# Kernel tuning notes

Hardware: AMD Instinct MI355X
Metric: run time of the kernel (lower is better)

The kernel has to match this reference:

```python
import jax, jax.numpy as jnp
import numpy as np

B, S, H = 2, 2048, 2048
NQ, NKV, DH = 16, 8, 128
EPS = 1e-6
ROPE_BASE = 10000.0


def setup_inputs() -> dict:
    key = jax.random.key(0)
    ks = jax.random.split(key, 6)
    hidden_states = jax.random.normal(ks[0], (B, S, H), dtype=jnp.float32)
    # real RoPE tables
    inv_freq = 1.0 / (ROPE_BASE ** (jnp.arange(0, DH, 2, dtype=jnp.float32) / DH))
    pos = jnp.arange(S, dtype=jnp.float32)
    freqs = pos[:, None] * inv_freq[None, :]              # [S, DH/2]
    emb = jnp.concatenate([freqs, freqs], axis=-1)        # [S, DH]
    cos = jnp.broadcast_to(jnp.cos(emb)[None], (B, S, DH))
    sin = jnp.broadcast_to(jnp.sin(emb)[None], (B, S, DH))
    # additive causal mask [1,1,S,S]
    causal = jnp.tril(jnp.ones((S, S), dtype=bool))
    attention_mask = jnp.where(causal, 0.0, jnp.finfo(jnp.float32).min)[None, None]
    q_w = jax.random.normal(ks[1], (H, H), dtype=jnp.float32) * 0.02
    k_w = jax.random.normal(ks[2], (NKV * DH, H), dtype=jnp.float32) * 0.02
    v_w = jax.random.normal(ks[3], (NKV * DH, H), dtype=jnp.float32) * 0.02
    o_w = jax.random.normal(ks[4], (H, H), dtype=jnp.float32) * 0.02
    return {"hidden_states": hidden_states, "cos": cos, "sin": sin,
            "attention_mask": attention_mask,
            "q_w": q_w, "k_w": k_w, "v_w": v_w, "o_w": o_w}


def _rotate_half(x):
    x1, x2 = jnp.split(x, 2, axis=-1)
    return jnp.concatenate([-x2, x1], axis=-1)


def _l2norm(x, eps=EPS):
    # weightless RMS norm over head_dim (Llama4TextL2Norm)
    return x * jax.lax.rsqrt(jnp.mean(x * x, axis=-1, keepdims=True) + eps)


def reference(hidden_states, cos, sin, attention_mask, q_w, k_w, v_w, o_w):
    b, s, _ = hidden_states.shape
    # projections (no bias) -> [B, n_heads, S, DH]
    q = jnp.einsum('bsh,dh->bsd', hidden_states, q_w).reshape(b, s, NQ, DH).transpose(0, 2, 1, 3)
    k = jnp.einsum('bsh,dh->bsd', hidden_states, k_w).reshape(b, s, NKV, DH).transpose(0, 2, 1, 3)
    v = jnp.einsum('bsh,dh->bsd', hidden_states, v_w).reshape(b, s, NKV, DH).transpose(0, 2, 1, 3)
    # NanoChat negates sin before standard HF rotary
    sin_e = (-sin)[:, None, :, :]   # [B,1,S,DH]
    cos_e = cos[:, None, :, :]
    q = q * cos_e + _rotate_half(q) * sin_e
    k = k * cos_e + _rotate_half(k) * sin_e
    # weightless QK RMS norm
    q = _l2norm(q)
    k = _l2norm(k)
    # GQA: repeat kv heads
    groups = NQ // NKV
    k = jnp.repeat(k, groups, axis=1)
    v = jnp.repeat(v, groups, axis=1)
    scaling = DH ** -0.5
    scores = jnp.einsum('bhqd,bhkd->bhqk', q, k) * scaling + attention_mask
    probs = jax.nn.softmax(scores, axis=-1)
    attn = jnp.einsum('bhqk,bhkd->bhqd', probs, v)           # [B,H,S,DH]
    attn = attn.transpose(0, 2, 1, 3).reshape(b, s, NQ * DH)
    out = jnp.einsum('bsd,hd->bsh', attn, o_w)
    return out
```

## Files before the change

### kernel.cpp

```cpp
#include <hip/hip_runtime.h>

typedef unsigned short ushort_t;
typedef __bf16 bf16x8 __attribute__((ext_vector_type(8)));
typedef float f32x4 __attribute__((ext_vector_type(4)));
typedef unsigned int u32x4 __attribute__((ext_vector_type(4)));
typedef unsigned short us4 __attribute__((ext_vector_type(4)));
typedef unsigned short us8 __attribute__((ext_vector_type(8)));

#define DEVINL __device__ __forceinline__

DEVINL ushort_t f2bf(float f) {
    unsigned u = __float_as_uint(f);
    u += 0x7FFF + ((u >> 16) & 1);
    return (ushort_t)(u >> 16);
}
DEVINL float bf2f(ushort_t h) { return __uint_as_float(((unsigned)h) << 16); }

DEVINL void gload_lds16(const void* g, void* l) {
    __builtin_amdgcn_global_load_lds(
        (const __attribute__((address_space(1))) void*)g,
        (__attribute__((address_space(3))) void*)l, 16, 0, 0);
}

DEVINL bf16x8 ld_frag(const ushort_t* p) {
    us8 v = *(const us8*)p;
    return __builtin_bit_cast(bf16x8, v);
}

#define BAR()     asm volatile("s_barrier" ::: "memory")
#define LGKM0()   asm volatile("s_waitcnt lgkmcnt(0)" ::: "memory")
#define VMCNT(n)  asm volatile("s_waitcnt vmcnt(" #n ")" ::: "memory")

#define BARRIER_KEEP4()  asm volatile("s_waitcnt vmcnt(4)\n\ts_barrier" ::: "memory")
#define BARRIER_KEEP0()  asm volatile("s_waitcnt vmcnt(0)\n\ts_barrier" ::: "memory")

__global__ __launch_bounds__(256) void convert_all(const f32x4* __restrict__ h,
                                                   const f32x4* __restrict__ qw,
                                                   const f32x4* __restrict__ kw,
                                                   const f32x4* __restrict__ vw,
                                                   const f32x4* __restrict__ ow,
                                                   us4* __restrict__ hb,
                                                   us4* __restrict__ wqkv,
                                                   us4* __restrict__ owb) {
    const int N0 = 2097152;
    const int N1 = 1048576;
    const int N2 = 524288;
    const int N3 = 524288;
    int i = blockIdx.x * 256 + threadIdx.x;
    const f32x4* src; us4* dst;
    if (i < N0)                               { src = h  + i;                 dst = hb + i; }
    else if ((i -= N0) < N1)                  { src = qw + i;                 dst = wqkv + i; }
    else if ((i -= N1) < N2)                  { src = kw + i;                 dst = wqkv + 1048576 + i; }
    else if ((i -= N2) < N3)                  { src = vw + i;                 dst = wqkv + 1572864 + i; }
    else                                      { i -= N3; src = ow + i;       dst = owb + i; }
    f32x4 f = *src;
    us4 o;
    o[0] = f2bf(f[0]); o[1] = f2bf(f[1]); o[2] = f2bf(f[2]); o[3] = f2bf(f[3]);
    *dst = o;
}

template <typename OutT>
__global__ __launch_bounds__(512, 2) void gemm256(const ushort_t* __restrict__ A,
                                                  const ushort_t* __restrict__ W,
                                                  OutT* __restrict__ C,
                                                  int N, int K) {
    __shared__ ushort_t As[2][256 * 64];
    __shared__ ushort_t Bs[2][256 * 64];
    const int t = threadIdx.x;
    const int lane = t & 63;
    const int quad = lane >> 4, l16 = lane & 15;
    const int wm = t >> 8, wn = (t >> 6) & 3;

    int bid = blockIdx.x;
    int xcd = bid & 7, j = bid >> 3;
    int tm, tn;
    if (N == 4096) { tm = (xcd >> 1) * 4 + (j >> 3); tn = (xcd & 1) * 8 + (j & 7); }
    else           { tm = xcd * 2 + (j >> 3);        tn = j & 7; }
    const int bm = tm * 256, bn = tn * 256;

    const int srow0 = t >> 3;
    const int sg0 = ((t & 7) ^ (srow0 & 7)) * 8;
    const int srow1 = srow0 + 64;
    const int sg1 = ((t & 7) ^ (srow1 & 7)) * 8;

    auto stageA = [&](int buf, int half, int k0) {
        gload_lds16(A + (size_t)(bm + half * 128 + srow0) * K + k0 + sg0,
                    &As[buf][half * 8192 + t * 8]);
        gload_lds16(A + (size_t)(bm + half * 128 + srow1) * K + k0 + sg1,
                    &As[buf][half * 8192 + 4096 + t * 8]);
    };
    auto stageB = [&](int buf, int half, int k0) {
        gload_lds16(W + (size_t)(bn + half * 128 + srow0) * K + k0 + sg0,
                    &Bs[buf][half * 8192 + t * 8]);
        gload_lds16(W + (size_t)(bn + half * 128 + srow1) * K + k0 + sg1,
                    &Bs[buf][half * 8192 + 4096 + t * 8]);
    };

    const int xsw = l16 & 7;
    const int arow = (wm * 128 + l16) * 64;
    const int brow = (wn * 64 + l16) * 64;
    const int ac0 = ((0 + quad) ^ xsw) * 8;
    const int ac1 = ((4 + quad) ^ xsw) * 8;

    auto ldA = [&](int buf, int mf, int kk) {
        return ld_frag(&As[buf][arow + mf * 1024 + (kk ? ac1 : ac0)]);
    };
    auto ldB = [&](int buf, int nf, int kk) {
        return ld_frag(&Bs[buf][brow + nf * 1024 + (kk ? ac1 : ac0)]);
    };

    f32x4 acc[8][4];
#pragma unroll
    for (int i = 0; i < 8; i++)
#pragma unroll
        for (int jj = 0; jj < 4; jj++) acc[i][jj] = f32x4{0.f, 0.f, 0.f, 0.f};

    const int NIT = K >> 6;
    stageA(0, 0, 0); stageA(0, 1, 0); stageB(0, 0, 0); stageB(0, 1, 0);
    VMCNT(4);
    stageB(1, 0, 64); stageB(1, 1, 64); stageA(1, 0, 64);
    VMCNT(6);
    BAR();

    bf16x8 a[4][2], b[4][2];
    for (int tt = 0; tt < NIT; ++tt) {
        const int buf = tt & 1;
        const int k2 = (tt + 2) << 6;

#pragma unroll
        for (int mt = 0; mt < 4; mt++) { a[mt][0] = ldA(buf, mt, 0); a[mt][1] = ldA(buf, mt, 1); }
#pragma unroll
        for (int nt = 0; nt < 4; nt++) { b[nt][0] = ldB(buf, nt, 0); b[nt][1] = ldB(buf, nt, 1); }
        if (tt + 1 < NIT) stageA(buf ^ 1, 1, (tt + 1) << 6);
        BAR(); LGKM0();
        __builtin_amdgcn_s_setprio(1);
#pragma unroll
        for (int mt = 0; mt < 4; mt++)
#pragma unroll
            for (int nt = 0; nt < 2; nt++)
#pragma unroll
                for (int kk = 0; kk < 2; kk++)
                    acc[mt][nt] = __builtin_amdgcn_mfma_f32_16x16x32_bf16(a[mt][kk], b[nt][kk], acc[mt][nt], 0, 0, 0);
        __builtin_amdgcn_s_setprio(0);
        LGKM0();
        BAR();

        if (tt + 2 < NIT) stageB(buf, 0, k2);
        BAR();
        __builtin_amdgcn_s_setprio(1);
#pragma unroll
        for (int mt = 0; mt < 4; mt++)
#pragma unroll
            for (int nt = 0; nt < 2; nt++)
#pragma unroll
                for (int kk = 0; kk < 2; kk++)
                    acc[mt][2 + nt] = __builtin_amdgcn_mfma_f32_16x16x32_bf16(a[mt][kk], b[2 + nt][kk], acc[mt][2 + nt], 0, 0, 0);
        __builtin_amdgcn_s_setprio(0);
        BAR();

#pragma unroll
        for (int mt = 0; mt < 4; mt++) { a[mt][0] = ldA(buf, 4 + mt, 0); a[mt][1] = ldA(buf, 4 + mt, 1); }
        if (tt + 2 < NIT) stageB(buf, 1, k2);
        BAR(); LGKM0();
        __builtin_amdgcn_s_setprio(1);
#pragma unroll
        for (int mt = 0; mt < 4; mt++)
#pragma unroll
            for (int nt = 0; nt < 2; nt++)
#pragma unroll
                for (int kk = 0; kk < 2; kk++)
                    acc[4 + mt][nt] = __builtin_amdgcn_mfma_f32_16x16x32_bf16(a[mt][kk], b[nt][kk], acc[4 + mt][nt], 0, 0, 0);
        __builtin_amdgcn_s_setprio(0);
        BAR();

        if (tt + 2 < NIT)      { stageA(buf, 0, k2); VMCNT(6); }
        else if (tt + 1 < NIT) { VMCNT(0); }
        BAR();
        __builtin_amdgcn_s_setprio(1);
#pragma unroll
        for (int mt = 0; mt < 4; mt++)
#pragma unroll
            for (int nt = 0; nt < 2; nt++)
#pragma unroll
                for (int kk = 0; kk < 2; kk++)
                    acc[4 + mt][2 + nt] = __builtin_amdgcn_mfma_f32_16x16x32_bf16(a[mt][kk], b[2 + nt][kk], acc[4 + mt][2 + nt], 0, 0, 0);
        __builtin_amdgcn_s_setprio(0);
        BAR();
    }

#pragma unroll
    for (int mf = 0; mf < 8; mf++)
#pragma unroll
        for (int nf = 0; nf < 4; nf++) {
            const int row = bm + wm * 128 + mf * 16 + quad * 4;
            const int col = bn + wn * 64 + nf * 16 + l16;
#pragma unroll
            for (int rr = 0; rr < 4; rr++) {
                float v = acc[mf][nf][rr];
                if constexpr (sizeof(OutT) == 2)
                    C[(size_t)(row + rr) * N + col] = (OutT)f2bf(v);
                else
                    C[(size_t)(row + rr) * N + col] = v;
            }
        }
}

__global__ __launch_bounds__(256) void rope_norm(const ushort_t* __restrict__ qkv,
                                                 const float* __restrict__ cosb,
                                                 const float* __restrict__ sinb,
                                                 ushort_t* __restrict__ q,
                                                 ushort_t* __restrict__ k) {
    int row = blockIdx.x;
    int b = row >> 11, s = row & 2047;
    int w = threadIdx.x >> 6, lane = threadIdx.x & 63;
    int hh = blockIdx.y * 4 + w;
    const ushort_t* src = qkv + (size_t)row * 4096 + hh * 128;
    float x1 = bf2f(src[lane]);
    float x2 = bf2f(src[lane + 64]);
    float c = cosb[(size_t)row * 128 + lane];
    float sn = sinb[(size_t)row * 128 + lane];
    float y1 = x1 * c + x2 * sn;
    float y2 = x2 * c - x1 * sn;
    float ss = y1 * y1 + y2 * y2;
#pragma unroll
    for (int off = 1; off < 64; off <<= 1) ss += __shfl_xor(ss, off);
    float rinv = rsqrtf(ss * (1.0f / 128.0f) + 1e-6f);
    y1 *= rinv; y2 *= rinv;
    ushort_t* dst;
    if (hh < 16) dst = q + (((size_t)(b * 16 + hh)) * 2048 + s) * 128;
    else         dst = k + (((size_t)(b * 8 + hh - 16)) * 2048 + s) * 128;
    dst[lane] = f2bf(y1);
    dst[lane + 64] = f2bf(y2);
}

__global__ __launch_bounds__(256) void v_transpose(const ushort_t* __restrict__ qkv,
                                                   ushort_t* __restrict__ vt) {
    __shared__ ushort_t tile[64 * 72];
    int t = threadIdx.x;
    int s0 = blockIdx.x * 64, d0 = blockIdx.y * 64, bh = blockIdx.z;
    int b = bh >> 3, kvh = bh & 7;
    {
        int sl = t >> 2, c = t & 3;
        const ushort_t* src = qkv + (size_t)(b * 2048 + s0 + sl) * 4096 + 3072 + kvh * 128 + d0 + c * 16;
        u32x4 v0 = *(const u32x4*)src;
        u32x4 v1 = *(const u32x4*)(src + 8);
        *(u32x4*)&tile[sl * 72 + c * 16] = v0;
        *(u32x4*)&tile[sl * 72 + c * 16 + 8] = v1;
    }
    __syncthreads();
    {
        int dl = t >> 2, c = t & 3;
        alignas(16) ushort_t tmp[16];
#pragma unroll
        for (int i = 0; i < 16; i++) tmp[i] = tile[(c * 16 + i) * 72 + dl];
        ushort_t* dst = vt + (size_t)(bh * 128 + d0 + dl) * 2048 + s0 + c * 16;
        *(u32x4*)dst = *(const u32x4*)&tmp[0];
        *(u32x4*)(dst + 8) = *(const u32x4*)&tmp[8];
    }
}

__global__ __launch_bounds__(512) void flash_attn(const ushort_t* __restrict__ q,
                                                  const ushort_t* __restrict__ k,
                                                  const ushort_t* __restrict__ vt,
                                                  ushort_t* __restrict__ attn) {
    __shared__ ushort_t Ks[3][4 * 64 * 32];
    __shared__ ushort_t Vts[3][2 * 128 * 32];
    __shared__ ushort_t Ps[2 * 64 * 72];
    __shared__ float    Lred[2][4][2][16];
    const int t = threadIdx.x;
    const int w = t >> 6, lane = t & 63;
    const int w4 = w & 3, wh = w >> 2;
    const int quad = lane >> 4, l16 = lane & 15;
    const int sw = (l16 >> 1) & 3;
    const int lid = blockIdx.x;
    const int xcd = lid & 7, jj = lid >> 3;
    const int g = xcd * 2 + (jj >> 4);
    const int p = jj & 15;
    const int b = g >> 3, kvh = g & 7;
    const int h0 = kvh * 2;
    const size_t kbase = ((size_t)(b * 8 + kvh)) * 2048 * 128;
    const size_t vbase = ((size_t)(b * 8 + kvh)) * 128 * 2048;

    const float C1 = 0.12751744f;
    const float C2 = 1.45f;

    auto stage = [&](int j0, int buf) {
#pragma unroll
        for (int i = 0; i < 2; i++) {
            int u = i * 512 + t;
            int qd = u >> 8, rr = (u >> 2) & 63;
            int c4 = ((u & 3) ^ ((rr >> 1) & 3)) * 8;
            gload_lds16(k + kbase + (size_t)(j0 + rr) * 128 + qd * 32 + c4,
                        (char*)Ks[buf] + u * 16);
        }
#pragma unroll
        for (int i = 0; i < 2; i++) {
            int u = i * 512 + t;
            int ks = u >> 9, dd = (u >> 2) & 127;
            int c4 = ((u & 3) ^ ((dd >> 1) & 3)) * 8;
            gload_lds16(vt + vbase + (size_t)dd * 2048 + j0 + ks * 32 + c4,
                        (char*)Vts[buf] + u * 16);
        }
    };

    const int qtile0 = 31 - p;
    const int S_total = qtile0 + 1 + p + 1;
    auto j0_of = [&](int s) { return (s <= qtile0 ? s : s - qtile0 - 1) * 64; };

    stage(j0_of(0), 0);
    stage(j0_of(1), 1);
    int sidx = 0, cb = 0, pb = 2;

    for (int pass = 0; pass < 2; ++pass) {
        const int qi = pass ? p : qtile0;
        const int q0 = qi * 64;

        bf16x8 qf[2][4];
#pragma unroll
        for (int h = 0; h < 2; h++) {
            const size_t qbase = ((size_t)(b * 16 + h0 + h) * 2048 + q0 + w4 * 16 + l16) * 128;
#pragma unroll
            for (int qd = 0; qd < 4; qd++) {
                us8 v = *(const us8*)(q + qbase + qd * 32 + quad * 8);
                qf[h][qd] = __builtin_bit_cast(bf16x8, v);
            }
        }

        f32x4 o[2][4];
#pragma unroll
        for (int h = 0; h < 2; h++)
#pragma unroll
            for (int i = 0; i < 4; i++) o[h][i] = f32x4{0.f, 0.f, 0.f, 0.f};
        float lsum[2][4];
#pragma unroll
        for (int h = 0; h < 2; h++)
#pragma unroll
            for (int r = 0; r < 4; r++) lsum[h][r] = 0.f;

        for (int jt = 0; jt <= qi; ++jt) {
            const int j0 = jt * 64;
            const bool diag = (jt == qi);
            if (sidx + 1 < S_total) BARRIER_KEEP4();
            else                    BARRIER_KEEP0();
            if (sidx + 2 < S_total) stage(j0_of(sidx + 2), pb);
            const ushort_t* Kb = Ks[cb];
            const ushort_t* Vb = Vts[cb];
            cb = cb == 2 ? 0 : cb + 1;
            pb = pb == 2 ? 0 : pb + 1;
            sidx++;

            f32x4 sc[2][2];
#pragma unroll
            for (int h = 0; h < 2; h++)
#pragma unroll
                for (int c = 0; c < 2; c++) sc[h][c] = f32x4{0.f, 0.f, 0.f, 0.f};
            __builtin_amdgcn_s_setprio(1);
#pragma unroll
            for (int c = 0; c < 2; c++)
#pragma unroll
                for (int qd = 0; qd < 4; qd++) {
                    bf16x8 kf = ld_frag(&Kb[qd * 2048 + ((wh * 2 + c) * 16 + l16) * 32 + (quad ^ sw) * 8]);
                    sc[0][c] = __builtin_amdgcn_mfma_f32_16x16x32_bf16(qf[0][qd], kf, sc[0][c], 0, 0, 0);
                    sc[1][c] = __builtin_amdgcn_mfma_f32_16x16x32_bf16(qf[1][qd], kf, sc[1][c], 0, 0, 0);
                }
            __builtin_amdgcn_s_setprio(0);

#pragma unroll
            for (int c = 0; c < 2; c++)
#pragma unroll
                for (int r = 0; r < 4; r++) {
                    float p0 = __builtin_amdgcn_exp2f(sc[0][c][r] * C1 - C2);
                    float p1 = __builtin_amdgcn_exp2f(sc[1][c][r] * C1 - C2);
                    if (diag) {
                        int kg = j0 + wh * 32 + c * 16 + l16;
                        int qg = q0 + w4 * 16 + quad * 4 + r;
                        if (kg > qg) { p0 = 0.f; p1 = 0.f; }
                    }
                    lsum[0][r] += p0;
                    lsum[1][r] += p1;
                    int prow = w4 * 16 + quad * 4 + r;
                    int pcol = wh * 32 + c * 16 + l16;
                    Ps[prow * 72 + pcol] = f2bf(p0);
                    Ps[4608 + prow * 72 + pcol] = f2bf(p1);
                }
            LGKM0();
            BAR();

            __builtin_amdgcn_s_setprio(1);
#pragma unroll
            for (int ks = 0; ks < 2; ks++) {
                bf16x8 pf0 = ld_frag(&Ps[(w4 * 16 + l16) * 72 + ks * 32 + quad * 8]);
                bf16x8 pf1 = ld_frag(&Ps[4608 + (w4 * 16 + l16) * 72 + ks * 32 + quad * 8]);
#pragma unroll
                for (int od = 0; od < 4; od++) {
                    bf16x8 vf = ld_frag(&Vb[ks * 4096 + (wh * 64 + od * 16 + l16) * 32 + (quad ^ sw) * 8]);
                    o[0][od] = __builtin_amdgcn_mfma_f32_16x16x32_bf16(pf0, vf, o[0][od], 0, 0, 0);
                    o[1][od] = __builtin_amdgcn_mfma_f32_16x16x32_bf16(pf1, vf, o[1][od], 0, 0, 0);
                }
            }
            __builtin_amdgcn_s_setprio(0);
        }

        float rl[2][4];
#pragma unroll
        for (int h = 0; h < 2; h++)
#pragma unroll
            for (int r = 0; r < 4; r++) {
                float s = lsum[h][r];
#pragma unroll
                for (int off = 1; off < 16; off <<= 1) s += __shfl_xor(s, off);
                if (l16 == 0) Lred[wh][w4][h][quad * 4 + r] = s;
            }
        LGKM0();
        BAR();
#pragma unroll
        for (int h = 0; h < 2; h++)
#pragma unroll
            for (int r = 0; r < 4; r++)
                rl[h][r] = 1.0f / (Lred[0][w4][h][quad * 4 + r] + Lred[1][w4][h][quad * 4 + r]);

#pragma unroll
        for (int h = 0; h < 2; h++) {
            const size_t obase = ((size_t)(b * 2048 + q0 + w4 * 16 + quad * 4)) * 2048
                                 + (h0 + h) * 128 + wh * 64;
#pragma unroll
            for (int od = 0; od < 4; od++)
#pragma unroll
                for (int r = 0; r < 4; r++)
                    attn[obase + (size_t)r * 2048 + od * 16 + l16] = f2bf(o[h][od][r] * rl[h][r]);
        }
    }
}

extern "C" void kernel_launch(void* const* d_in, const int* in_sizes, int n_in,
                              void* d_out, int out_size, void* d_ws, size_t ws_size,
                              hipStream_t stream) {
    (void)in_sizes; (void)n_in; (void)out_size; (void)ws_size;
    const float* hidden = (const float*)d_in[0];
    const float* cosb   = (const float*)d_in[1];
    const float* sinb   = (const float*)d_in[2];
    const float* q_w    = (const float*)d_in[4];
    const float* k_w    = (const float*)d_in[5];
    const float* v_w    = (const float*)d_in[6];
    const float* o_w    = (const float*)d_in[7];

    char* ws = (char*)d_ws;
    ushort_t* hb   = (ushort_t*)(ws);
    ushort_t* wqkv = (ushort_t*)(ws + (16ull << 20));
    ushort_t* owb  = (ushort_t*)(ws + (32ull << 20));
    ushort_t* qkv  = (ushort_t*)(ws + (40ull << 20));
    ushort_t* attn = qkv;
    ushort_t* qb   = (ushort_t*)(ws + (72ull << 20));
    ushort_t* kb   = (ushort_t*)(ws + (88ull << 20));
    ushort_t* vt   = (ushort_t*)(ws + (96ull << 20));

    convert_all<<<20480, 256, 0, stream>>>((const f32x4*)hidden, (const f32x4*)q_w,
                                           (const f32x4*)k_w, (const f32x4*)v_w,
                                           (const f32x4*)o_w,
                                           (us4*)hb, (us4*)wqkv, (us4*)owb);

    gemm256<ushort_t><<<256, 512, 0, stream>>>(hb, wqkv, qkv, 4096, 2048);
    rope_norm<<<dim3(4096, 6), 256, 0, stream>>>(qkv, cosb, sinb, qb, kb);
    v_transpose<<<dim3(32, 2, 16), 256, 0, stream>>>(qkv, vt);
    flash_attn<<<256, 512, 0, stream>>>(qb, kb, vt, attn);
    gemm256<float><<<128, 512, 0, stream>>>(attn, owb, (float*)d_out, 2048, 2048);
}
```

Before: 349.8 us.

## Restructure flash attention around 32x32 MFMA with in-register P and split-K reduction

Rewrites the attention inner loop to use 32x32x16 bf16 MFMAs. S^T is computed so the probabilities can be packed to bf16 with v_cvt_pk_bf16 and permlane32 swaps, which keeps P in registers and removes the LDS round-trip and the mid-iteration barrier for P. Waves are repartitioned so each wave owns one head and a 32-row query chunk over half of the KV tile, and the two KV halves are reduced through LDS at the end of each pass. The LDS pipeline drops from triple to double buffering with a full vmcnt drain each iteration, and launch bounds now request 2 blocks per CU. This may expose more load latency in exchange for less LDS traffic and fewer barriers.

```diff
diff --git a/kernel.cpp b/kernel.cpp
--- a/kernel.cpp
+++ b/kernel.cpp
@@ -3,6 +3,7 @@
 typedef unsigned short ushort_t;
 typedef __bf16 bf16x8 __attribute__((ext_vector_type(8)));
 typedef float f32x4 __attribute__((ext_vector_type(4)));
+typedef float f32x16 __attribute__((ext_vector_type(16)));
 typedef unsigned int u32x4 __attribute__((ext_vector_type(4)));
 typedef unsigned short us4 __attribute__((ext_vector_type(4)));
 typedef unsigned short us8 __attribute__((ext_vector_type(8)));
@@ -27,12 +28,17 @@
     return __builtin_bit_cast(bf16x8, v);
 }
 
+DEVINL unsigned cvt_pk_bf16(float a, float b) {
+    unsigned r;
+    asm("v_cvt_pk_bf16_f32 %0, %1, %2" : "=v"(r) : "v"(a), "v"(b));
+    return r;
+}
+#define PERMSWAP(a, b) asm volatile("v_permlane32_swap_b32 %0, %1" : "+v"(a), "+v"(b))
+
 #define BAR()     asm volatile("s_barrier" ::: "memory")
 #define LGKM0()   asm volatile("s_waitcnt lgkmcnt(0)" ::: "memory")
 #define VMCNT(n)  asm volatile("s_waitcnt vmcnt(" #n ")" ::: "memory")
-
-#define BARRIER_KEEP4()  asm volatile("s_waitcnt vmcnt(4)\n\ts_barrier" ::: "memory")
-#define BARRIER_KEEP0()  asm volatile("s_waitcnt vmcnt(0)\n\ts_barrier" ::: "memory")
+#define BARRIER_DRAIN() asm volatile("s_waitcnt vmcnt(0)\n\ts_barrier" ::: "memory")
 
 __global__ __launch_bounds__(256) void convert_all(const f32x4* __restrict__ h,
                                                    const f32x4* __restrict__ qw,
@@ -259,19 +265,20 @@
     }
 }
 
-__global__ __launch_bounds__(512) void flash_attn(const ushort_t* __restrict__ q,
-                                                  const ushort_t* __restrict__ k,
-                                                  const ushort_t* __restrict__ vt,
-                                                  ushort_t* __restrict__ attn) {
-    __shared__ ushort_t Ks[3][4 * 64 * 32];
-    __shared__ ushort_t Vts[3][2 * 128 * 32];
-    __shared__ ushort_t Ps[2 * 64 * 72];
-    __shared__ float    Lred[2][4][2][16];
+__global__ __launch_bounds__(512, 2) void flash_attn(const ushort_t* __restrict__ q,
+                                                     const ushort_t* __restrict__ k,
+                                                     const ushort_t* __restrict__ vt,
+                                                     ushort_t* __restrict__ attn) {
+    __shared__ ushort_t Ks[2][4 * 64 * 32];
+    __shared__ ushort_t Vts[2][2 * 128 * 32];
+    __shared__ float    Om[4][16][64][4];
+    __shared__ float    Ls[2][4][32];
     const int t = threadIdx.x;
     const int w = t >> 6, lane = t & 63;
-    const int w4 = w & 3, wh = w >> 2;
-    const int quad = lane >> 4, l16 = lane & 15;
-    const int sw = (l16 >> 1) & 3;
+    const int wh = w & 1, chunk = (w >> 1) & 1, wk = w >> 2;
+    const int pid = chunk * 2 + wh;
+    const int l31 = lane & 31, hi = lane >> 5;
+    const int swz = (l31 >> 1) & 3;
     const int lid = blockIdx.x;
     const int xcd = lid & 7, jj = lid >> 3;
     const int g = xcd * 2 + (jj >> 4);
@@ -308,126 +315,129 @@
     auto j0_of = [&](int s) { return (s <= qtile0 ? s : s - qtile0 - 1) * 64; };
 
     stage(j0_of(0), 0);
-    stage(j0_of(1), 1);
-    int sidx = 0, cb = 0, pb = 2;
+    int sidx = 0;
 
     for (int pass = 0; pass < 2; ++pass) {
         const int qi = pass ? p : qtile0;
         const int q0 = qi * 64;
-
-        bf16x8 qf[2][4];
-#pragma unroll
-        for (int h = 0; h < 2; h++) {
-            const size_t qbase = ((size_t)(b * 16 + h0 + h) * 2048 + q0 + w4 * 16 + l16) * 128;
-#pragma unroll
-            for (int qd = 0; qd < 4; qd++) {
-                us8 v = *(const us8*)(q + qbase + qd * 32 + quad * 8);
-                qf[h][qd] = __builtin_bit_cast(bf16x8, v);
-            }
-        }
-
-        f32x4 o[2][4];
-#pragma unroll
-        for (int h = 0; h < 2; h++)
-#pragma unroll
-            for (int i = 0; i < 4; i++) o[h][i] = f32x4{0.f, 0.f, 0.f, 0.f};
-        float lsum[2][4];
-#pragma unroll
-        for (int h = 0; h < 2; h++)
-#pragma unroll
-            for (int r = 0; r < 4; r++) lsum[h][r] = 0.f;
+        const int hgl = h0 + wh;
+        const int qg = q0 + chunk * 32 + l31;
+
+        bf16x8 qf[8];
+        {
+            const size_t qrow = ((size_t)(b * 16 + hgl) * 2048 + qg) * 128;
+#pragma unroll
+            for (int s = 0; s < 8; s++) {
+                us8 v = *(const us8*)(q + qrow + s * 16 + hi * 8);
+                qf[s] = __builtin_bit_cast(bf16x8, v);
+            }
+        }
+
+        f32x16 o[4];
+#pragma unroll
+        for (int i = 0; i < 4; i++)
+#pragma unroll
+            for (int r = 0; r < 16; r++) o[i][r] = 0.f;
+        float lsum = 0.f;
 
         for (int jt = 0; jt <= qi; ++jt) {
             const int j0 = jt * 64;
             const bool diag = (jt == qi);
-            if (sidx + 1 < S_total) BARRIER_KEEP4();
-            else                    BARRIER_KEEP0();
-            if (sidx + 2 < S_total) stage(j0_of(sidx + 2), pb);
-            const ushort_t* Kb = Ks[cb];
-            const ushort_t* Vb = Vts[cb];
-            cb = cb == 2 ? 0 : cb + 1;
-            pb = pb == 2 ? 0 : pb + 1;
+            const int buf = sidx & 1;
+            BARRIER_DRAIN();
+            if (sidx + 1 < S_total) stage(j0_of(sidx + 1), buf ^ 1);
             sidx++;
 
-            f32x4 sc[2][2];
-#pragma unroll
-            for (int h = 0; h < 2; h++)
-#pragma unroll
-                for (int c = 0; c < 2; c++) sc[h][c] = f32x4{0.f, 0.f, 0.f, 0.f};
+            f32x16 sc;
+#pragma unroll
+            for (int r = 0; r < 16; r++) sc[r] = 0.f;
             __builtin_amdgcn_s_setprio(1);
 #pragma unroll
-            for (int c = 0; c < 2; c++)
-#pragma unroll
-                for (int qd = 0; qd < 4; qd++) {
-                    bf16x8 kf = ld_frag(&Kb[qd * 2048 + ((wh * 2 + c) * 16 + l16) * 32 + (quad ^ sw) * 8]);
-                    sc[0][c] = __builtin_amdgcn_mfma_f32_16x16x32_bf16(qf[0][qd], kf, sc[0][c], 0, 0, 0);
-                    sc[1][c] = __builtin_amdgcn_mfma_f32_16x16x32_bf16(qf[1][qd], kf, sc[1][c], 0, 0, 0);
+            for (int s = 0; s < 8; s++) {
+                bf16x8 kf = ld_frag(&Ks[buf][(s >> 1) * 2048 + (wk * 32 + l31) * 32 +
+                                             (((((s & 1) << 1) | hi)) ^ swz) * 8]);
+                sc = __builtin_amdgcn_mfma_f32_32x32x16_bf16(kf, qf[s], sc, 0, 0, 0);
+            }
+            __builtin_amdgcn_s_setprio(0);
+
+#pragma unroll
+            for (int r = 0; r < 16; r++)
+                sc[r] = __builtin_amdgcn_exp2f(sc[r] * C1 - C2);
+            if (diag) {
+                const int kvb = j0 + wk * 32 + 4 * hi;
+#pragma unroll
+                for (int r = 0; r < 16; r++) {
+                    int kg = kvb + (r & 3) + 8 * (r >> 2);
+                    if (kg > qg) sc[r] = 0.f;
+                }
+            }
+#pragma unroll
+            for (int r = 0; r < 16; r++) lsum += sc[r];
+
+            bf16x8 pf[2];
+#pragma unroll
+            for (int kp = 0; kp < 2; kp++) {
+                const int rb = kp * 8;
+                unsigned x0 = cvt_pk_bf16(sc[rb + 0], sc[rb + 1]);
+                unsigned x1 = cvt_pk_bf16(sc[rb + 2], sc[rb + 3]);
+                unsigned y0 = cvt_pk_bf16(sc[rb + 4], sc[rb + 5]);
+                unsigned y1 = cvt_pk_bf16(sc[rb + 6], sc[rb + 7]);
+                PERMSWAP(x0, y0);
+                PERMSWAP(x1, y1);
+                u32x4 pv; pv[0] = x0; pv[1] = x1; pv[2] = y0; pv[3] = y1;
+                pf[kp] = __builtin_bit_cast(bf16x8, pv);
+            }
+
+            __builtin_amdgcn_s_setprio(1);
+#pragma unroll
+            for (int kp = 0; kp < 2; kp++)
+#pragma unroll
+                for (int od = 0; od < 4; od++) {
+                    bf16x8 vf = ld_frag(&Vts[buf][wk * 4096 + (od * 32 + l31) * 32 +
+                                                  ((((kp << 1) | hi)) ^ swz) * 8]);
+                    o[od] = __builtin_amdgcn_mfma_f32_32x32x16_bf16(pf[kp], vf, o[od], 0, 0, 0);
                 }
             __builtin_amdgcn_s_setprio(0);
-
-#pragma unroll
-            for (int c = 0; c < 2; c++)
-#pragma unroll
-                for (int r = 0; r < 4; r++) {
-                    float p0 = __builtin_amdgcn_exp2f(sc[0][c][r] * C1 - C2);
-                    float p1 = __builtin_amdgcn_exp2f(sc[1][c][r] * C1 - C2);
-                    if (diag) {
-                        int kg = j0 + wh * 32 + c * 16 + l16;
-                        int qg = q0 + w4 * 16 + quad * 4 + r;
-                        if (kg > qg) { p0 = 0.f; p1 = 0.f; }
-                    }
-                    lsum[0][r] += p0;
-                    lsum[1][r] += p1;
-                    int prow = w4 * 16 + quad * 4 + r;
-                    int pcol = wh * 32 + c * 16 + l16;
-                    Ps[prow * 72 + pcol] = f2bf(p0);
-                    Ps[4608 + prow * 72 + pcol] = f2bf(p1);
+        }
+
+        lsum += __shfl_xor(lsum, 32);
+        if (hi == 0) Ls[wk][pid][l31] = lsum;
+        if (wk == 1) {
+#pragma unroll
+            for (int od = 0; od < 4; od++)
+#pragma unroll
+                for (int r4 = 0; r4 < 4; r4++) {
+                    f32x4 v;
+                    v[0] = o[od][r4 * 4 + 0]; v[1] = o[od][r4 * 4 + 1];
+                    v[2] = o[od][r4 * 4 + 2]; v[3] = o[od][r4 * 4 + 3];
+                    *(f32x4*)&Om[pid][od * 4 + r4][lane][0] = v;
                 }
-            LGKM0();
-            BAR();
-
-            __builtin_amdgcn_s_setprio(1);
-#pragma unroll
-            for (int ks = 0; ks < 2; ks++) {
-                bf16x8 pf0 = ld_frag(&Ps[(w4 * 16 + l16) * 72 + ks * 32 + quad * 8]);
-                bf16x8 pf1 = ld_frag(&Ps[4608 + (w4 * 16 + l16) * 72 + ks * 32 + quad * 8]);
-#pragma unroll
-                for (int od = 0; od < 4; od++) {
-                    bf16x8 vf = ld_frag(&Vb[ks * 4096 + (wh * 64 + od * 16 + l16) * 32 + (quad ^ sw) * 8]);
-                    o[0][od] = __builtin_amdgcn_mfma_f32_16x16x32_bf16(pf0, vf, o[0][od], 0, 0, 0);
-                    o[1][od] = __builtin_amdgcn_mfma_f32_16x16x32_bf16(pf1, vf, o[1][od], 0, 0, 0);
+        }
+        LGKM0();
+        BAR();
+        if (wk == 0) {
+#pragma unroll
+            for (int od = 0; od < 4; od++)
+#pragma unroll
+                for (int r4 = 0; r4 < 4; r4++) {
+                    f32x4 m = *(const f32x4*)&Om[pid][od * 4 + r4][lane][0];
+                    o[od][r4 * 4 + 0] += m[0]; o[od][r4 * 4 + 1] += m[1];
+                    o[od][r4 * 4 + 2] += m[2]; o[od][r4 * 4 + 3] += m[3];
                 }
-            }
-            __builtin_amdgcn_s_setprio(0);
-        }
-
-        float rl[2][4];
-#pragma unroll
-        for (int h = 0; h < 2; h++)
-#pragma unroll
-            for (int r = 0; r < 4; r++) {
-                float s = lsum[h][r];
-#pragma unroll
-                for (int off = 1; off < 16; off <<= 1) s += __shfl_xor(s, off);
-                if (l16 == 0) Lred[wh][w4][h][quad * 4 + r] = s;
-            }
-        LGKM0();
-        BAR();
-#pragma unroll
-        for (int h = 0; h < 2; h++)
-#pragma unroll
-            for (int r = 0; r < 4; r++)
-                rl[h][r] = 1.0f / (Lred[0][w4][h][quad * 4 + r] + Lred[1][w4][h][quad * 4 + r]);
-
-#pragma unroll
-        for (int h = 0; h < 2; h++) {
-            const size_t obase = ((size_t)(b * 2048 + q0 + w4 * 16 + quad * 4)) * 2048
-                                 + (h0 + h) * 128 + wh * 64;
+            float rl[16];
+#pragma unroll
+            for (int r = 0; r < 16; r++) {
+                int ql = (r & 3) + 8 * (r >> 2) + 4 * hi;
+                rl[r] = 1.0f / (Ls[0][pid][ql] + Ls[1][pid][ql]);
+            }
 #pragma unroll
             for (int od = 0; od < 4; od++)
 #pragma unroll
-                for (int r = 0; r < 4; r++)
-                    attn[obase + (size_t)r * 2048 + od * 16 + l16] = f2bf(o[h][od][r] * rl[h][r]);
+                for (int r = 0; r < 16; r++) {
+                    int qg2 = q0 + chunk * 32 + (r & 3) + 8 * (r >> 2) + 4 * hi;
+                    attn[(size_t)(b * 2048 + qg2) * 2048 + hgl * 128 + od * 32 + l31] =
+                        f2bf(o[od][r] * rl[r]);
+                }
         }
     }
 }
```

After: 336.3 us. 1.04x faster.
